# Performance work log

Hardware: AMD Instinct MI355X
Metric: run time of the kernel (lower is better)

The kernel has to match this reference:

```python
import jax, jax.numpy as jnp
import numpy as np

N = 50000
EPS = 1e-12


def sage_conv(x, src, dst, Wl, bl, Wr):
    # mean aggregation of source features into target nodes
    msg = x[src]                                            # [E, d]
    agg = jax.ops.segment_sum(msg, dst, num_segments=N)     # [N, d]
    cnt = jax.ops.segment_sum(jnp.ones_like(src, dtype=x.dtype), dst, num_segments=N)
    agg = agg / jnp.maximum(cnt, 1.0)[:, None]
    out = agg @ Wl + bl + x @ Wr                            # lin_l(aggr) + lin_r(x)
    # L2 normalize (PyG normalize=True)
    nrm = jnp.maximum(jnp.linalg.norm(out, axis=-1, keepdims=True), EPS)
    return out / nrm


def setup_inputs() -> dict:
    key = jax.random.key(0)
    ks = jax.random.split(key, 12)
    d_in, d_h, d_out = 128, 128, 40
    E = 800000
    x = jax.random.normal(ks[0], (N, d_in), dtype=jnp.float32)
    edge_index = jax.random.randint(ks[1], (2, E), 0, N, dtype=jnp.int64)

    def xavier(k, shp):
        lim = np.sqrt(6.0 / (shp[0] + shp[1]))
        return jax.random.uniform(k, shp, jnp.float32, -lim, lim)

    return {
        "x": x, "edge_index": edge_index,
        "W1l": xavier(ks[2], (d_in, d_h)), "b1": jnp.zeros((d_h,), jnp.float32), "W1r": xavier(ks[3], (d_in, d_h)),
        "W2l": xavier(ks[4], (d_h, d_h)),  "b2": jnp.zeros((d_h,), jnp.float32), "W2r": xavier(ks[5], (d_h, d_h)),
        "W3l": xavier(ks[6], (d_h, d_h)),  "b3": jnp.zeros((d_h,), jnp.float32), "W3r": xavier(ks[7], (d_h, d_h)),
        "Wfc": xavier(ks[8], (d_h, d_out)), "bfc": jnp.zeros((d_out,), jnp.float32),
    }


def reference(x, edge_index, W1l, b1, W1r, W2l, b2, W2r, W3l, b3, W3r, Wfc, bfc):
    src, dst = edge_index[0], edge_index[1]
    h = sage_conv(x, src, dst, W1l, b1, W1r)
    h = jax.nn.relu(h)                       # dropout = identity at eval
    h = sage_conv(h, src, dst, W2l, b2, W2r)
    h = jax.nn.relu(h)
    h = sage_conv(h, src, dst, W3l, b3, W3r)
    return jax.nn.softmax(h @ Wfc + bfc, axis=-1)
```

## Files before the change

### kernel.cpp

```cpp
#include <hip/hip_runtime.h>
#include <math.h>

#define NN 50000
#define D 128
#define NB 49
#define NBUK 256
#define EPB 4096

typedef __attribute__((ext_vector_type(8))) short bf16x8;
typedef __attribute__((ext_vector_type(4))) float f32x4;
typedef __attribute__((ext_vector_type(2))) float f32x2;

__device__ __forceinline__ float bf2f(unsigned short u) {
    union { unsigned int i; float f; } c;
    c.i = ((unsigned int)u) << 16;
    return c.f;
}
__device__ __forceinline__ unsigned short f2bf(float f) {
    union { float f; unsigned int i; } c;
    c.f = f;
    unsigned int u = c.i;
    return (unsigned short)((u + 0x7FFFu + ((u >> 16) & 1u)) >> 16);
}
__device__ __forceinline__ unsigned char f2f8(float v) {
    return (unsigned char)(__builtin_amdgcn_cvt_pk_fp8_f32(v, v, 0, false) & 0xFF);
}


__global__ __launch_bounds__(256) void f32_cvt_kernel(const float* __restrict__ src,
                                                      unsigned short* __restrict__ dstb,
                                                      unsigned int* __restrict__ dst8,
                                                      int n4) {
    int i = blockIdx.x * 256 + threadIdx.x;
    if (i < n4) {
        float4 v = ((const float4*)src)[i];
        ushort4 o;
        o.x = f2bf(v.x); o.y = f2bf(v.y); o.z = f2bf(v.z); o.w = f2bf(v.w);
        ((ushort4*)dstb)[i] = o;
        unsigned int p01 = __builtin_amdgcn_cvt_pk_fp8_f32(v.x, v.y, 0, false);
        unsigned int p23 = __builtin_amdgcn_cvt_pk_fp8_f32(v.z, v.w, 0, false);
        dst8[i] = (p01 & 0xFFFFu) | (p23 << 16);
    }
}


__global__ __launch_bounds__(256) void pack_all_kernel(const float* __restrict__ W0,
                                                       const float* __restrict__ W1,
                                                       const float* __restrict__ W2,
                                                       const float* __restrict__ W3,
                                                       const float* __restrict__ W4,
                                                       const float* __restrict__ W5,
                                                       unsigned short* __restrict__ P) {
    int i = blockIdx.x * 256 + threadIdx.x;
    int w = i >> 14, j = i & 16383;
    const float* W = (w == 0) ? W0 : (w == 1) ? W1 : (w == 2) ? W2
                   : (w == 3) ? W3 : (w == 4) ? W4 : W5;
    int e = j & 7, l = (j >> 3) & 63, n = (j >> 9) & 7, ks = j >> 12;
    int k = ks * 32 + (l >> 4) * 8 + e;
    int col = n * 16 + (l & 15);
    P[i] = f2bf(W[k * D + col]);
}


__global__ __launch_bounds__(256) void bucket_hist_kernel(const int* __restrict__ e, int E,
                                                          int* __restrict__ bukcnt) {
    __shared__ int h[NBUK];
    int t = threadIdx.x;
    h[t] = 0;
    __syncthreads();
    int base = blockIdx.x * EPB;
    #pragma unroll
    for (int k = 0; k < 4; ++k) {
        int idx = base + k * 1024 + t * 4;
        if (idx + 4 <= E) {
            int4 d = *(const int4*)(e + E + idx);
            atomicAdd(&h[d.x >> 8], 1);
            atomicAdd(&h[d.y >> 8], 1);
            atomicAdd(&h[d.z >> 8], 1);
            atomicAdd(&h[d.w >> 8], 1);
        } else {
            for (int i = idx; i < E; ++i) atomicAdd(&h[e[E + i] >> 8], 1);
        }
    }
    __syncthreads();
    if (h[t]) atomicAdd(&bukcnt[t], h[t]);
}

__global__ __launch_bounds__(256) void bucket_scan_kernel(const int* __restrict__ bukcnt,
                                                          int* __restrict__ bukbase,
                                                          int* __restrict__ bukfill, int E) {
    __shared__ int wsum[4], woff[4];
    int t = threadIdx.x;
    int lane = t & 63, wave = t >> 6;
    int v = bukcnt[t];
    int incl = v;
    for (int off = 1; off < 64; off <<= 1) {
        int u = __shfl_up(incl, off);
        if (lane >= off) incl += u;
    }
    if (lane == 63) wsum[wave] = incl;
    __syncthreads();
    if (t == 0) {
        int r = 0;
        #pragma unroll
        for (int w = 0; w < 4; ++w) { woff[w] = r; r += wsum[w]; }
    }
    __syncthreads();
    int excl = woff[wave] + incl - v;
    bukbase[t] = excl;
    bukfill[t] = excl;
    if (t == 255) bukbase[NBUK] = E;
}

__global__ __launch_bounds__(256) void bucket_scatter_kernel(const int* __restrict__ e, int E,
                                                             int* __restrict__ bukfill,
                                                             unsigned int* __restrict__ ebuk) {
    __shared__ int h[NBUK];
    __shared__ int res[NBUK];
    int t = threadIdx.x;
    h[t] = 0;
    __syncthreads();
    int base = blockIdx.x * EPB;
    int4 d[4];
    #pragma unroll
    for (int k = 0; k < 4; ++k) {
        int idx = base + k * 1024 + t * 4;
        if (idx + 4 <= E) {
            d[k] = *(const int4*)(e + E + idx);
        } else {
            d[k].x = (idx + 0 < E) ? e[E + idx + 0] : -1;
            d[k].y = (idx + 1 < E) ? e[E + idx + 1] : -1;
            d[k].z = (idx + 2 < E) ? e[E + idx + 2] : -1;
            d[k].w = (idx + 3 < E) ? e[E + idx + 3] : -1;
        }
        if (d[k].x >= 0) atomicAdd(&h[d[k].x >> 8], 1);
        if (d[k].y >= 0) atomicAdd(&h[d[k].y >> 8], 1);
        if (d[k].z >= 0) atomicAdd(&h[d[k].z >> 8], 1);
        if (d[k].w >= 0) atomicAdd(&h[d[k].w >> 8], 1);
    }
    __syncthreads();
    res[t] = h[t] ? atomicAdd(&bukfill[t], h[t]) : 0;
    h[t] = 0;
    __syncthreads();
    #pragma unroll
    for (int k = 0; k < 4; ++k) {
        int idx = base + k * 1024 + t * 4;
        int4 s;
        if (idx + 4 <= E) {
            s = *(const int4*)(e + idx);
        } else {
            s.x = (idx + 0 < E) ? e[idx + 0] : 0;
            s.y = (idx + 1 < E) ? e[idx + 1] : 0;
            s.z = (idx + 2 < E) ? e[idx + 2] : 0;
            s.w = (idx + 3 < E) ? e[idx + 3] : 0;
        }
        if (d[k].x >= 0) { int b = d[k].x >> 8; int r = atomicAdd(&h[b], 1);
            ebuk[res[b] + r] = (unsigned int)(s.x & 0xFFFF) | ((unsigned int)(d[k].x & 255) << 16); }
        if (d[k].y >= 0) { int b = d[k].y >> 8; int r = atomicAdd(&h[b], 1);
            ebuk[res[b] + r] = (unsigned int)(s.y & 0xFFFF) | ((unsigned int)(d[k].y & 255) << 16); }
        if (d[k].z >= 0) { int b = d[k].z >> 8; int r = atomicAdd(&h[b], 1);
            ebuk[res[b] + r] = (unsigned int)(s.z & 0xFFFF) | ((unsigned int)(d[k].z & 255) << 16); }
        if (d[k].w >= 0) { int b = d[k].w >> 8; int r = atomicAdd(&h[b], 1);
            ebuk[res[b] + r] = (unsigned int)(s.w & 0xFFFF) | ((unsigned int)(d[k].w & 255) << 16); }
    }
}

__global__ __launch_bounds__(256) void cnt_hist_kernel(const unsigned int* __restrict__ ebuk,
                                                       const int* __restrict__ bukbase,
                                                       int* __restrict__ cnt, int N) {
    __shared__ int c[NBUK];
    int t = threadIdx.x, b = blockIdx.x;
    c[t] = 0;
    __syncthreads();
    int lo = bukbase[b], hi = bukbase[b + 1];
    for (int i = lo + t; i < hi; i += 256) atomicAdd(&c[ebuk[i] >> 16], 1);
    __syncthreads();
    int g = b * NBUK + t;
    if (g < N) cnt[g] = c[t];
}

__global__ __launch_bounds__(256) void scan_blocks_kernel(const int* __restrict__ cnt,
                                                          int* __restrict__ row_ptr,
                                                          int* __restrict__ bsum, int N) {
    __shared__ int wsum[4], woff[4];
    int t = threadIdx.x;
    int lane = t & 63, wave = t >> 6;
    int base = blockIdx.x * 1024 + t * 4;
    int4 v = make_int4(0, 0, 0, 0);
    if (base + 4 <= N) v = *(const int4*)(cnt + base);
    int s = v.x + v.y + v.z + v.w;
    int incl = s;
    for (int off = 1; off < 64; off <<= 1) {
        int u = __shfl_up(incl, off);
        if (lane >= off) incl += u;
    }
    if (lane == 63) wsum[wave] = incl;
    __syncthreads();
    if (t == 0) {
        int r = 0;
        #pragma unroll
        for (int w = 0; w < 4; ++w) { woff[w] = r; r += wsum[w]; }
    }
    __syncthreads();
    int excl = woff[wave] + incl - s;
    if (base + 4 <= N) {
        int4 rp;
        rp.x = excl;
        rp.y = rp.x + v.x;
        rp.z = rp.y + v.y;
        rp.w = rp.z + v.z;
        *(int4*)(row_ptr + base) = rp;
    }
    if (t == 255) bsum[blockIdx.x] = woff[3] + wsum[3];
}

__global__ __launch_bounds__(64) void scan_bsums_kernel(int* __restrict__ bsum, int nb) {
    int l = threadIdx.x;
    int v = (l < nb) ? bsum[l] : 0;
    int incl = v;
    for (int off = 1; off < 64; off <<= 1) {
        int u = __shfl_up(incl, off);
        if (l >= off) incl += u;
    }
    if (l < nb) bsum[l] = incl - v;
}

__global__ __launch_bounds__(256) void scan_add_kernel(const int* __restrict__ cnt,
                                                       int* __restrict__ row_ptr,
                                                       const int* __restrict__ bsum,
                                                       float* __restrict__ inv_cnt,
                                                       int N, int E) {
    int base = blockIdx.x * 1024 + threadIdx.x * 4;
    int off = bsum[blockIdx.x];
    if (base + 4 <= N) {
        int4 rp = *(int4*)(row_ptr + base);
        rp.x += off; rp.y += off; rp.z += off; rp.w += off;
        *(int4*)(row_ptr + base) = rp;
        int4 c = *(const int4*)(cnt + base);
        float4 ic;
        ic.x = 1.0f / fmaxf((float)c.x, 1.0f);
        ic.y = 1.0f / fmaxf((float)c.y, 1.0f);
        ic.z = 1.0f / fmaxf((float)c.z, 1.0f);
        ic.w = 1.0f / fmaxf((float)c.w, 1.0f);
        *(float4*)(inv_cnt + base) = ic;
    }
    if (blockIdx.x == 0 && threadIdx.x == 0) row_ptr[N] = E;
}

__global__ __launch_bounds__(256) void csr_scatter_kernel(const unsigned int* __restrict__ ebuk,
                                                          const int* __restrict__ bukbase,
                                                          const int* __restrict__ row_ptr,
                                                          unsigned short* __restrict__ csr_src,
                                                          int N) {
    __shared__ int rp[NBUK];
    __shared__ int lf[NBUK];
    int t = threadIdx.x, b = blockIdx.x;
    int g = b * NBUK + t;
    rp[t] = (g < N) ? row_ptr[g] : 0;
    lf[t] = 0;
    __syncthreads();
    int lo = bukbase[b], hi = bukbase[b + 1];
    for (int i = lo + t; i < hi; i += 256) {
        unsigned int v = ebuk[i];
        int dl = v >> 16;
        int r = atomicAdd(&lf[dl], 1);
        csr_src[rp[dl] + r] = (unsigned short)(v & 0xFFFF);
    }
}


__device__ __forceinline__ void acc_f8(float& x, float& y, float& z, float& w,
                                       unsigned int v) {
    f32x2 lo = __builtin_amdgcn_cvt_pk_f32_fp8(v, false);
    f32x2 hi = __builtin_amdgcn_cvt_pk_f32_fp8(v, true);
    x += lo.x; y += lo.y; z += hi.x; w += hi.y;
}

__global__ __launch_bounds__(256) void aggregate_kernel(const unsigned int* __restrict__ h8,
                                                        const int* __restrict__ row_ptr,
                                                        const unsigned short* __restrict__ csr_src,
                                                        const float* __restrict__ inv_cnt,
                                                        unsigned short* __restrict__ agg, int N) {
    int node = (int)((blockIdx.x * blockDim.x + threadIdx.x) >> 5);
    int l = threadIdx.x & 31;
    if (node >= N) return;
    int beg = row_ptr[node], end = row_ptr[node + 1];
    float a0x = 0.f, a0y = 0.f, a0z = 0.f, a0w = 0.f;
    float a1x = 0.f, a1y = 0.f, a1z = 0.f, a1w = 0.f;
    for (int base = beg; base < end; base += 32) {
        int idx = 0;
        if (base + l < end) idx = csr_src[base + l];
        int n = min(32, end - base);
        int j = 0;
        for (; j + 8 <= n; j += 8) {
            int s0 = __shfl(idx, j + 0, 32);
            int s1 = __shfl(idx, j + 1, 32);
            int s2 = __shfl(idx, j + 2, 32);
            int s3 = __shfl(idx, j + 3, 32);
            int s4 = __shfl(idx, j + 4, 32);
            int s5 = __shfl(idx, j + 5, 32);
            int s6 = __shfl(idx, j + 6, 32);
            int s7 = __shfl(idx, j + 7, 32);
            unsigned int v0 = h8[(size_t)s0 * 32 + l];
            unsigned int v1 = h8[(size_t)s1 * 32 + l];
            unsigned int v2 = h8[(size_t)s2 * 32 + l];
            unsigned int v3 = h8[(size_t)s3 * 32 + l];
            unsigned int v4 = h8[(size_t)s4 * 32 + l];
            unsigned int v5 = h8[(size_t)s5 * 32 + l];
            unsigned int v6 = h8[(size_t)s6 * 32 + l];
            unsigned int v7 = h8[(size_t)s7 * 32 + l];
            acc_f8(a0x, a0y, a0z, a0w, v0);
            acc_f8(a1x, a1y, a1z, a1w, v1);
            acc_f8(a0x, a0y, a0z, a0w, v2);
            acc_f8(a1x, a1y, a1z, a1w, v3);
            acc_f8(a0x, a0y, a0z, a0w, v4);
            acc_f8(a1x, a1y, a1z, a1w, v5);
            acc_f8(a0x, a0y, a0z, a0w, v6);
            acc_f8(a1x, a1y, a1z, a1w, v7);
        }
        for (; j < n; ++j) {
            int s = __shfl(idx, j, 32);
            acc_f8(a0x, a0y, a0z, a0w, h8[(size_t)s * 32 + l]);
        }
    }
    float iv = inv_cnt[node];
    ushort4 o;
    o.x = f2bf((a0x + a1x) * iv);
    o.y = f2bf((a0y + a1y) * iv);
    o.z = f2bf((a0z + a1z) * iv);
    o.w = f2bf((a0w + a1w) * iv);
    ((ushort4*)agg)[(size_t)node * 32 + l] = o;
}


__global__ __launch_bounds__(256) void sage_mfma_kernel(const unsigned short* __restrict__ aggb,
                                                        const unsigned short* __restrict__ xb,
                                                        const unsigned short* __restrict__ wlp,
                                                        const unsigned short* __restrict__ wrp,
                                                        const float* __restrict__ bl,
                                                        unsigned short* __restrict__ outb,
                                                        unsigned char* __restrict__ out8,
                                                        float* __restrict__ outf,
                                                        int relu, int N) {
    int t = threadIdx.x;
    int w = t >> 6;
    int l = t & 63;
    int rlo = l & 15;
    int khi = l >> 4;
    int row0 = blockIdx.x * 64 + w * 16;
    int rowA = row0 + rlo;
    bool okA = rowA < N;

    f32x4 acc[8];
    #pragma unroll
    for (int n = 0; n < 8; ++n) {
        float b = bl[n * 16 + rlo];
        acc[n] = (f32x4){b, b, b, b};
    }

    const short* Ap = (const short*)aggb + (size_t)(okA ? rowA : 0) * D + khi * 8;
    const short* Xp = (const short*)xb   + (size_t)(okA ? rowA : 0) * D + khi * 8;
    const short* WL = (const short*)wlp + l * 8;
    const short* WR = (const short*)wrp + l * 8;
    const bf16x8 Z = {0, 0, 0, 0, 0, 0, 0, 0};

    #pragma unroll 1
    for (int ks = 0; ks < 4; ++ks) {
        bf16x8 a = okA ? *(const bf16x8*)(Ap + ks * 32) : Z;
        #pragma unroll
        for (int n = 0; n < 8; ++n) {
            bf16x8 b = *(const bf16x8*)(WL + (ks * 8 + n) * 512);
            acc[n] = __builtin_amdgcn_mfma_f32_16x16x32_bf16(a, b, acc[n], 0, 0, 0);
        }
    }
    #pragma unroll 1
    for (int ks = 0; ks < 4; ++ks) {
        bf16x8 a = okA ? *(const bf16x8*)(Xp + ks * 32) : Z;
        #pragma unroll
        for (int n = 0; n < 8; ++n) {
            bf16x8 b = *(const bf16x8*)(WR + (ks * 8 + n) * 512);
            acc[n] = __builtin_amdgcn_mfma_f32_16x16x32_bf16(a, b, acc[n], 0, 0, 0);
        }
    }

    #pragma unroll
    for (int r = 0; r < 4; ++r) {
        float s = 0.f;
        #pragma unroll
        for (int n = 0; n < 8; ++n) s += acc[n][r] * acc[n][r];
        s += __shfl_xor(s, 1);
        s += __shfl_xor(s, 2);
        s += __shfl_xor(s, 4);
        s += __shfl_xor(s, 8);
        float inv = 1.0f / fmaxf(sqrtf(s), 1e-12f);
        int gr = row0 + khi * 4 + r;
        if (gr < N) {
            if (outb) {
                #pragma unroll
                for (int n = 0; n < 8; ++n) {
                    float v = acc[n][r] * inv;
                    if (relu) v = fmaxf(v, 0.f);
                    outb[(size_t)gr * D + n * 16 + rlo] = f2bf(v);
                    out8[(size_t)gr * D + n * 16 + rlo] = f2f8(v);
                }
            } else {
                #pragma unroll
                for (int n = 0; n < 8; ++n) {
                    float v = acc[n][r] * inv;
                    outf[(size_t)gr * D + n * 16 + rlo] = v;
                }
            }
        }
    }
}


__global__ __launch_bounds__(256, 4) void fc_softmax_kernel(const float* __restrict__ h,
                                                            const float* __restrict__ Wfc,
                                                            const float* __restrict__ bfc,
                                                            float* __restrict__ out, int N) {
    __shared__ float sH[32 * 132];
    __shared__ float sW[128 * 40];
    __shared__ float sB[40];
    int t = threadIdx.x;
    int row0 = blockIdx.x * 32;

    const float4* W4 = (const float4*)Wfc;
    float4* sW4 = (float4*)sW;
    for (int i = t; i < 1280; i += 256) sW4[i] = W4[i];
    if (t < 40) sB[t] = bfc[t];

    const float4* h4 = (const float4*)h;
    for (int i = t; i < 32 * 32; i += 256) {
        int r = i >> 5, c = i & 31;
        int gr = row0 + r;
        float4 v = make_float4(0.f, 0.f, 0.f, 0.f);
        if (gr < N) v = h4[(size_t)gr * 32 + c];
        *(float4*)(sH + r * 132 + c * 4) = v;
    }
    __syncthreads();

    int r = t >> 3, sub = t & 7;
    int c0 = sub * 5;
    float acc[5];
    #pragma unroll
    for (int i = 0; i < 5; ++i) acc[i] = sB[c0 + i];

    const float* hr = sH + r * 132;
    for (int k = 0; k < 128; ++k) {
        float hv = hr[k];
        const float* wk = sW + k * 40 + c0;
        #pragma unroll
        for (int i = 0; i < 5; ++i) acc[i] += hv * wk[i];
    }

    float m = acc[0];
    #pragma unroll
    for (int i = 1; i < 5; ++i) m = fmaxf(m, acc[i]);
    for (int off = 1; off < 8; off <<= 1) m = fmaxf(m, __shfl_xor(m, off));
    float s = 0.f;
    #pragma unroll
    for (int i = 0; i < 5; ++i) { acc[i] = expf(acc[i] - m); s += acc[i]; }
    for (int off = 1; off < 8; off <<= 1) s += __shfl_xor(s, off);
    float inv = 1.0f / s;

    int gr = row0 + r;
    if (gr < N) {
        #pragma unroll
        for (int i = 0; i < 5; ++i) out[(size_t)gr * 40 + c0 + i] = acc[i] * inv;
    }
}


extern "C" void kernel_launch(void* const* d_in, const int* in_sizes, int n_in,
                              void* d_out, int out_size, void* d_ws, size_t ws_size,
                              hipStream_t stream) {
    const float* x   = (const float*)d_in[0];
    const int*   e   = (const int*)d_in[1];
    const float* W1l = (const float*)d_in[2];
    const float* b1  = (const float*)d_in[3];
    const float* W1r = (const float*)d_in[4];
    const float* W2l = (const float*)d_in[5];
    const float* b2  = (const float*)d_in[6];
    const float* W2r = (const float*)d_in[7];
    const float* W3l = (const float*)d_in[8];
    const float* b3  = (const float*)d_in[9];
    const float* W3r = (const float*)d_in[10];
    const float* Wfc = (const float*)d_in[11];
    const float* bfc = (const float*)d_in[12];
    float* out = (float*)d_out;

    const int N = NN;
    const int E = in_sizes[1] / 2;

    unsigned char* p = (unsigned char*)d_ws;
    unsigned short* xb   = (unsigned short*)p; p += (size_t)N * D * 2;
    unsigned short* h1b  = (unsigned short*)p; p += (size_t)N * D * 2;
    unsigned short* h2b  = (unsigned short*)p; p += (size_t)N * D * 2;
    unsigned short* aggb = (unsigned short*)p; p += (size_t)N * D * 2;
    unsigned char*  xf8  = (unsigned char*)p;  p += (size_t)N * D;
    unsigned char*  h1f8 = (unsigned char*)p;  p += (size_t)N * D;
    unsigned short* wpk  = (unsigned short*)p; p += 6 * 16384 * 2;
    float* inv_cnt = (float*)p; p += (size_t)N * 4;
    int* row_ptr = (int*)p; p += (size_t)(N + 4) * 4;
    int* cnt     = (int*)p; p += (size_t)N * 4;
    int* bukcnt  = (int*)p; p += NBUK * 4;
    int* bukbase = (int*)p; p += (NBUK + 4) * 4;
    int* bukfill = (int*)p; p += NBUK * 4;
    int* bsum    = (int*)p; p += 64 * 4;
    unsigned int* ebuk = (unsigned int*)p; p += (size_t)E * 4;
    unsigned short* csr_src = (unsigned short*)p;
    float* h3f = (float*)xb;
    unsigned char* h2f8 = xf8;

    unsigned short* w1lp = wpk;
    unsigned short* w1rp = wpk + 16384;
    unsigned short* w2lp = wpk + 2 * 16384;
    unsigned short* w2rp = wpk + 3 * 16384;
    unsigned short* w3lp = wpk + 4 * 16384;
    unsigned short* w3rp = wpk + 5 * 16384;

    hipMemsetAsync(bukcnt, 0, sizeof(int) * NBUK, stream);

    f32_cvt_kernel<<<(N * D / 4 + 255) / 256, 256, 0, stream>>>(x, xb, (unsigned int*)xf8,
                                                                N * D / 4);
    pack_all_kernel<<<384, 256, 0, stream>>>(W1l, W1r, W2l, W2r, W3l, W3r, wpk);

    int EB = (E + EPB - 1) / EPB;
    bucket_hist_kernel<<<EB, 256, 0, stream>>>(e, E, bukcnt);
    bucket_scan_kernel<<<1, 256, 0, stream>>>(bukcnt, bukbase, bukfill, E);
    bucket_scatter_kernel<<<EB, 256, 0, stream>>>(e, E, bukfill, ebuk);
    cnt_hist_kernel<<<NBUK, 256, 0, stream>>>(ebuk, bukbase, cnt, N);
    scan_blocks_kernel<<<NB, 256, 0, stream>>>(cnt, row_ptr, bsum, N);
    scan_bsums_kernel<<<1, 64, 0, stream>>>(bsum, NB);
    scan_add_kernel<<<NB, 256, 0, stream>>>(cnt, row_ptr, bsum, inv_cnt, N, E);
    csr_scatter_kernel<<<NBUK, 256, 0, stream>>>(ebuk, bukbase, row_ptr, csr_src, N);

    int aggBlocks = (N * 32 + 255) / 256;
    int sageBlocks = (N + 63) / 64;
    int fcBlocks = (N + 31) / 32;

    aggregate_kernel<<<aggBlocks, 256, 0, stream>>>((const unsigned int*)xf8, row_ptr,
                                                    csr_src, inv_cnt, aggb, N);
    sage_mfma_kernel<<<sageBlocks, 256, 0, stream>>>(aggb, xb, w1lp, w1rp, b1,
                                                     h1b, h1f8, nullptr, 1, N);

    aggregate_kernel<<<aggBlocks, 256, 0, stream>>>((const unsigned int*)h1f8, row_ptr,
                                                    csr_src, inv_cnt, aggb, N);
    sage_mfma_kernel<<<sageBlocks, 256, 0, stream>>>(aggb, h1b, w2lp, w2rp, b2,
                                                     h2b, h2f8, nullptr, 1, N);

    aggregate_kernel<<<aggBlocks, 256, 0, stream>>>((const unsigned int*)h2f8, row_ptr,
                                                    csr_src, inv_cnt, aggb, N);
    sage_mfma_kernel<<<sageBlocks, 256, 0, stream>>>(aggb, h2b, w3lp, w3rp, b3,
                                                     nullptr, nullptr, h3f, 0, N);

    fc_softmax_kernel<<<fcBlocks, 256, 0, stream>>>(h3f, Wfc, bfc, out, N);
}
```

Baseline: 204.0 us.

## Fuse preprocessing kernels, merge count/scan, and fold FC softmax into last SAGE layer

Merges the x conversion and weight packing into one launch. Replaces the separate count histogram and three-pass scan with a per-bucket count and local scan, using the bucket base as the offset. Fuses the final SAGE layer's normalized output straight into shared memory, where the FC and softmax run without the fp32 round trip to global memory. This cuts several kernel launches and about 25 MB of intermediate traffic, at the cost of more shared memory (about 54 KB) in the fused kernel, which may lower occupancy.

```diff
diff --git a/kernel.cpp b/kernel.cpp
--- a/kernel.cpp
+++ b/kernel.cpp
@@ -3,7 +3,6 @@
 
 #define NN 50000
 #define D 128
-#define NB 49
 #define NBUK 256
 #define EPB 4096
 
@@ -27,38 +26,38 @@
 }
 
 
-__global__ __launch_bounds__(256) void f32_cvt_kernel(const float* __restrict__ src,
-                                                      unsigned short* __restrict__ dstb,
-                                                      unsigned int* __restrict__ dst8,
-                                                      int n4) {
-    int i = blockIdx.x * 256 + threadIdx.x;
-    if (i < n4) {
-        float4 v = ((const float4*)src)[i];
-        ushort4 o;
-        o.x = f2bf(v.x); o.y = f2bf(v.y); o.z = f2bf(v.z); o.w = f2bf(v.w);
-        ((ushort4*)dstb)[i] = o;
-        unsigned int p01 = __builtin_amdgcn_cvt_pk_fp8_f32(v.x, v.y, 0, false);
-        unsigned int p23 = __builtin_amdgcn_cvt_pk_fp8_f32(v.z, v.w, 0, false);
-        dst8[i] = (p01 & 0xFFFFu) | (p23 << 16);
-    }
-}
-
-
-__global__ __launch_bounds__(256) void pack_all_kernel(const float* __restrict__ W0,
-                                                       const float* __restrict__ W1,
-                                                       const float* __restrict__ W2,
-                                                       const float* __restrict__ W3,
-                                                       const float* __restrict__ W4,
-                                                       const float* __restrict__ W5,
-                                                       unsigned short* __restrict__ P) {
-    int i = blockIdx.x * 256 + threadIdx.x;
-    int w = i >> 14, j = i & 16383;
-    const float* W = (w == 0) ? W0 : (w == 1) ? W1 : (w == 2) ? W2
-                   : (w == 3) ? W3 : (w == 4) ? W4 : W5;
-    int e = j & 7, l = (j >> 3) & 63, n = (j >> 9) & 7, ks = j >> 12;
-    int k = ks * 32 + (l >> 4) * 8 + e;
-    int col = n * 16 + (l & 15);
-    P[i] = f2bf(W[k * D + col]);
+__global__ __launch_bounds__(256) void cvtpack_kernel(const float* __restrict__ x,
+                                                      unsigned short* __restrict__ xb,
+                                                      unsigned int* __restrict__ x8,
+                                                      int n4,
+                                                      const float* __restrict__ W0,
+                                                      const float* __restrict__ W1,
+                                                      const float* __restrict__ W2,
+                                                      const float* __restrict__ W3,
+                                                      const float* __restrict__ W4,
+                                                      const float* __restrict__ W5,
+                                                      unsigned short* __restrict__ P) {
+    if (blockIdx.x < 384) {
+        int i = blockIdx.x * 256 + threadIdx.x;
+        int w = i >> 14, j = i & 16383;
+        const float* W = (w == 0) ? W0 : (w == 1) ? W1 : (w == 2) ? W2
+                       : (w == 3) ? W3 : (w == 4) ? W4 : W5;
+        int e = j & 7, l = (j >> 3) & 63, n = (j >> 9) & 7, ks = j >> 12;
+        int k = ks * 32 + (l >> 4) * 8 + e;
+        int col = n * 16 + (l & 15);
+        P[i] = f2bf(W[k * D + col]);
+    } else {
+        int i = (blockIdx.x - 384) * 256 + threadIdx.x;
+        if (i < n4) {
+            float4 v = ((const float4*)x)[i];
+            ushort4 o;
+            o.x = f2bf(v.x); o.y = f2bf(v.y); o.z = f2bf(v.z); o.w = f2bf(v.w);
+            ((ushort4*)xb)[i] = o;
+            unsigned int p01 = __builtin_amdgcn_cvt_pk_fp8_f32(v.x, v.y, 0, false);
+            unsigned int p23 = __builtin_amdgcn_cvt_pk_fp8_f32(v.z, v.w, 0, false);
+            x8[i] = (p01 & 0xFFFFu) | (p23 << 16);
+        }
+    }
 }
 
 
@@ -165,31 +164,23 @@
     }
 }
 
-__global__ __launch_bounds__(256) void cnt_hist_kernel(const unsigned int* __restrict__ ebuk,
+
+__global__ __launch_bounds__(256) void cnt_scan_kernel(const unsigned int* __restrict__ ebuk,
                                                        const int* __restrict__ bukbase,
-                                                       int* __restrict__ cnt, int N) {
+                                                       int* __restrict__ row_ptr,
+                                                       float* __restrict__ inv_cnt,
+                                                       int N, int E) {
     __shared__ int c[NBUK];
+    __shared__ int wsum[4], woff[4];
     int t = threadIdx.x, b = blockIdx.x;
     c[t] = 0;
     __syncthreads();
     int lo = bukbase[b], hi = bukbase[b + 1];
     for (int i = lo + t; i < hi; i += 256) atomicAdd(&c[ebuk[i] >> 16], 1);
     __syncthreads();
-    int g = b * NBUK + t;
-    if (g < N) cnt[g] = c[t];
-}
-
-__global__ __launch_bounds__(256) void scan_blocks_kernel(const int* __restrict__ cnt,
-                                                          int* __restrict__ row_ptr,
-                                                          int* __restrict__ bsum, int N) {
-    __shared__ int wsum[4], woff[4];
-    int t = threadIdx.x;
+    int v = c[t];
     int lane = t & 63, wave = t >> 6;
-    int base = blockIdx.x * 1024 + t * 4;
-    int4 v = make_int4(0, 0, 0, 0);
-    if (base + 4 <= N) v = *(const int4*)(cnt + base);
-    int s = v.x + v.y + v.z + v.w;
-    int incl = s;
+    int incl = v;
     for (int off = 1; off < 64; off <<= 1) {
         int u = __shfl_up(incl, off);
         if (lane >= off) incl += u;
@@ -202,49 +193,13 @@
         for (int w = 0; w < 4; ++w) { woff[w] = r; r += wsum[w]; }
     }
     __syncthreads();
-    int excl = woff[wave] + incl - s;
-    if (base + 4 <= N) {
-        int4 rp;
-        rp.x = excl;
-        rp.y = rp.x + v.x;
-        rp.z = rp.y + v.y;
-        rp.w = rp.z + v.z;
-        *(int4*)(row_ptr + base) = rp;
-    }
-    if (t == 255) bsum[blockIdx.x] = woff[3] + wsum[3];
-}
-
-__global__ __launch_bounds__(64) void scan_bsums_kernel(int* __restrict__ bsum, int nb) {
-    int l = threadIdx.x;
-    int v = (l < nb) ? bsum[l] : 0;
-    int incl = v;
-    for (int off = 1; off < 64; off <<= 1) {
-        int u = __shfl_up(incl, off);
-        if (l >= off) incl += u;
-    }
-    if (l < nb) bsum[l] = incl - v;
-}
-
-__global__ __launch_bounds__(256) void scan_add_kernel(const int* __restrict__ cnt,
-                                                       int* __restrict__ row_ptr,
-                                                       const int* __restrict__ bsum,
-                                                       float* __restrict__ inv_cnt,
-                                                       int N, int E) {
-    int base = blockIdx.x * 1024 + threadIdx.x * 4;
-    int off = bsum[blockIdx.x];
-    if (base + 4 <= N) {
-        int4 rp = *(int4*)(row_ptr + base);
-        rp.x += off; rp.y += off; rp.z += off; rp.w += off;
-        *(int4*)(row_ptr + base) = rp;
-        int4 c = *(const int4*)(cnt + base);
-        float4 ic;
-        ic.x = 1.0f / fmaxf((float)c.x, 1.0f);
-        ic.y = 1.0f / fmaxf((float)c.y, 1.0f);
-        ic.z = 1.0f / fmaxf((float)c.z, 1.0f);
-        ic.w = 1.0f / fmaxf((float)c.w, 1.0f);
-        *(float4*)(inv_cnt + base) = ic;
-    }
-    if (blockIdx.x == 0 && threadIdx.x == 0) row_ptr[N] = E;
+    int excl = woff[wave] + incl - v;
+    int g = b * NBUK + t;
+    if (g < N) {
+        row_ptr[g] = bukbase[b] + excl;
+        inv_cnt[g] = 1.0f / fmaxf((float)v, 1.0f);
+    }
+    if (g == N) row_ptr[N] = E;
 }
 
 __global__ __launch_bounds__(256) void csr_scatter_kernel(const unsigned int* __restrict__ ebuk,
@@ -340,8 +295,7 @@
                                                         const float* __restrict__ bl,
                                                         unsigned short* __restrict__ outb,
                                                         unsigned char* __restrict__ out8,
-                                                        float* __restrict__ outf,
-                                                        int relu, int N) {
+                                                        int N) {
     int t = threadIdx.x;
     int w = t >> 6;
     int l = t & 63;
@@ -395,79 +349,121 @@
         float inv = 1.0f / fmaxf(sqrtf(s), 1e-12f);
         int gr = row0 + khi * 4 + r;
         if (gr < N) {
-            if (outb) {
-                #pragma unroll
-                for (int n = 0; n < 8; ++n) {
-                    float v = acc[n][r] * inv;
-                    if (relu) v = fmaxf(v, 0.f);
-                    outb[(size_t)gr * D + n * 16 + rlo] = f2bf(v);
-                    out8[(size_t)gr * D + n * 16 + rlo] = f2f8(v);
-                }
-            } else {
-                #pragma unroll
-                for (int n = 0; n < 8; ++n) {
-                    float v = acc[n][r] * inv;
-                    outf[(size_t)gr * D + n * 16 + rlo] = v;
-                }
+            #pragma unroll
+            for (int n = 0; n < 8; ++n) {
+                float v = fmaxf(acc[n][r] * inv, 0.f);
+                outb[(size_t)gr * D + n * 16 + rlo] = f2bf(v);
+                out8[(size_t)gr * D + n * 16 + rlo] = f2f8(v);
             }
         }
     }
 }
 
 
-__global__ __launch_bounds__(256, 4) void fc_softmax_kernel(const float* __restrict__ h,
-                                                            const float* __restrict__ Wfc,
-                                                            const float* __restrict__ bfc,
-                                                            float* __restrict__ out, int N) {
-    __shared__ float sH[32 * 132];
+__global__ __launch_bounds__(256) void sage_mfma_fc_kernel(const unsigned short* __restrict__ aggb,
+                                                           const unsigned short* __restrict__ xb,
+                                                           const unsigned short* __restrict__ wlp,
+                                                           const unsigned short* __restrict__ wrp,
+                                                           const float* __restrict__ bl,
+                                                           const float* __restrict__ Wfc,
+                                                           const float* __restrict__ bfc,
+                                                           float* __restrict__ out, int N) {
+    __shared__ float sH[64 * 132];
     __shared__ float sW[128 * 40];
     __shared__ float sB[40];
     int t = threadIdx.x;
-    int row0 = blockIdx.x * 32;
-
-    const float4* W4 = (const float4*)Wfc;
-    float4* sW4 = (float4*)sW;
-    for (int i = t; i < 1280; i += 256) sW4[i] = W4[i];
-    if (t < 40) sB[t] = bfc[t];
-
-    const float4* h4 = (const float4*)h;
-    for (int i = t; i < 32 * 32; i += 256) {
-        int r = i >> 5, c = i & 31;
-        int gr = row0 + r;
-        float4 v = make_float4(0.f, 0.f, 0.f, 0.f);
-        if (gr < N) v = h4[(size_t)gr * 32 + c];
-        *(float4*)(sH + r * 132 + c * 4) = v;
-    }
-    __syncthreads();
-
-    int r = t >> 3, sub = t & 7;
-    int c0 = sub * 5;
-    float acc[5];
-    #pragma unroll
-    for (int i = 0; i < 5; ++i) acc[i] = sB[c0 + i];
-
-    const float* hr = sH + r * 132;
+    int w = t >> 6;
+    int l = t & 63;
+    int rlo = l & 15;
+    int khi = l >> 4;
+    int row0 = blockIdx.x * 64 + w * 16;
+    int rowA = row0 + rlo;
+    bool okA = rowA < N;
+
+    {
+        const float4* W4 = (const float4*)Wfc;
+        float4* sW4 = (float4*)sW;
+        for (int i = t; i < 1280; i += 256) sW4[i] = W4[i];
+        if (t < 40) sB[t] = bfc[t];
+    }
+
+    f32x4 acc[8];
+    #pragma unroll
+    for (int n = 0; n < 8; ++n) {
+        float b = bl[n * 16 + rlo];
+        acc[n] = (f32x4){b, b, b, b};
+    }
+
+    const short* Ap = (const short*)aggb + (size_t)(okA ? rowA : 0) * D + khi * 8;
+    const short* Xp = (const short*)xb   + (size_t)(okA ? rowA : 0) * D + khi * 8;
+    const short* WL = (const short*)wlp + l * 8;
+    const short* WR = (const short*)wrp + l * 8;
+    const bf16x8 Z = {0, 0, 0, 0, 0, 0, 0, 0};
+
+    #pragma unroll 1
+    for (int ks = 0; ks < 4; ++ks) {
+        bf16x8 a = okA ? *(const bf16x8*)(Ap + ks * 32) : Z;
+        #pragma unroll
+        for (int n = 0; n < 8; ++n) {
+            bf16x8 b = *(const bf16x8*)(WL + (ks * 8 + n) * 512);
+            acc[n] = __builtin_amdgcn_mfma_f32_16x16x32_bf16(a, b, acc[n], 0, 0, 0);
+        }
+    }
+    #pragma unroll 1
+    for (int ks = 0; ks < 4; ++ks) {
+        bf16x8 a = okA ? *(const bf16x8*)(Xp + ks * 32) : Z;
+        #pragma unroll
+        for (int n = 0; n < 8; ++n) {
+            bf16x8 b = *(const bf16x8*)(WR + (ks * 8 + n) * 512);
+            acc[n] = __builtin_amdgcn_mfma_f32_16x16x32_bf16(a, b, acc[n], 0, 0, 0);
+        }
+    }
+
+    #pragma unroll
+    for (int r = 0; r < 4; ++r) {
+        float s = 0.f;
+        #pragma unroll
+        for (int n = 0; n < 8; ++n) s += acc[n][r] * acc[n][r];
+        s += __shfl_xor(s, 1);
+        s += __shfl_xor(s, 2);
+        s += __shfl_xor(s, 4);
+        s += __shfl_xor(s, 8);
+        float inv = 1.0f / fmaxf(sqrtf(s), 1e-12f);
+        int lr = w * 16 + khi * 4 + r;
+        #pragma unroll
+        for (int n = 0; n < 8; ++n)
+            sH[lr * 132 + n * 16 + rlo] = acc[n][r] * inv;
+    }
+    __syncthreads();
+
+    int r2 = t >> 2, sub = t & 3;
+    int c0 = sub * 10;
+    float fa[10];
+    #pragma unroll
+    for (int i = 0; i < 10; ++i) fa[i] = sB[c0 + i];
+    const float* hr = sH + r2 * 132;
     for (int k = 0; k < 128; ++k) {
         float hv = hr[k];
         const float* wk = sW + k * 40 + c0;
         #pragma unroll
-        for (int i = 0; i < 5; ++i) acc[i] += hv * wk[i];
-    }
-
-    float m = acc[0];
-    #pragma unroll
-    for (int i = 1; i < 5; ++i) m = fmaxf(m, acc[i]);
-    for (int off = 1; off < 8; off <<= 1) m = fmaxf(m, __shfl_xor(m, off));
-    float s = 0.f;
-    #pragma unroll
-    for (int i = 0; i < 5; ++i) { acc[i] = expf(acc[i] - m); s += acc[i]; }
-    for (int off = 1; off < 8; off <<= 1) s += __shfl_xor(s, off);
-    float inv = 1.0f / s;
-
-    int gr = row0 + r;
+        for (int i = 0; i < 10; ++i) fa[i] += hv * wk[i];
+    }
+    float m = fa[0];
+    #pragma unroll
+    for (int i = 1; i < 10; ++i) m = fmaxf(m, fa[i]);
+    m = fmaxf(m, __shfl_xor(m, 1));
+    m = fmaxf(m, __shfl_xor(m, 2));
+    float ssum = 0.f;
+    #pragma unroll
+    for (int i = 0; i < 10; ++i) { fa[i] = expf(fa[i] - m); ssum += fa[i]; }
+    ssum += __shfl_xor(ssum, 1);
+    ssum += __shfl_xor(ssum, 2);
+    float inv = 1.0f / ssum;
+
+    int gr = blockIdx.x * 64 + r2;
     if (gr < N) {
         #pragma unroll
-        for (int i = 0; i < 5; ++i) out[(size_t)gr * 40 + c0 + i] = acc[i] * inv;
+        for (int i = 0; i < 10; ++i) out[(size_t)gr * 40 + c0 + i] = fa[i] * inv;
     }
 }
 
@@ -503,14 +499,11 @@
     unsigned short* wpk  = (unsigned short*)p; p += 6 * 16384 * 2;
     float* inv_cnt = (float*)p; p += (size_t)N * 4;
     int* row_ptr = (int*)p; p += (size_t)(N + 4) * 4;
-    int* cnt     = (int*)p; p += (size_t)N * 4;
     int* bukcnt  = (int*)p; p += NBUK * 4;
     int* bukbase = (int*)p; p += (NBUK + 4) * 4;
     int* bukfill = (int*)p; p += NBUK * 4;
-    int* bsum    = (int*)p; p += 64 * 4;
     unsigned int* ebuk = (unsigned int*)p; p += (size_t)E * 4;
     unsigned short* csr_src = (unsigned short*)p;
-    float* h3f = (float*)xb;
     unsigned char* h2f8 = xf8;
 
     unsigned short* w1lp = wpk;
@@ -522,38 +515,32 @@
 
     hipMemsetAsync(bukcnt, 0, sizeof(int) * NBUK, stream);
 
-    f32_cvt_kernel<<<(N * D / 4 + 255) / 256, 256, 0, stream>>>(x, xb, (unsigned int*)xf8,
-                                                                N * D / 4);
-    pack_all_kernel<<<384, 256, 0, stream>>>(W1l, W1r, W2l, W2r, W3l, W3r, wpk);
+    int n4 = N * D / 4;
+    cvtpack_kernel<<<384 + (n4 + 255) / 256, 256, 0, stream>>>(
+        x, xb, (unsigned int*)xf8, n4, W1l, W1r, W2l, W2r, W3l, W3r, wpk);
 
     int EB = (E + EPB - 1) / EPB;
     bucket_hist_kernel<<<EB, 256, 0, stream>>>(e, E, bukcnt);
     bucket_scan_kernel<<<1, 256, 0, stream>>>(bukcnt, bukbase, bukfill, E);
     bucket_scatter_kernel<<<EB, 256, 0, stream>>>(e, E, bukfill, ebuk);
-    cnt_hist_kernel<<<NBUK, 256, 0, stream>>>(ebuk, bukbase, cnt, N);
-    scan_blocks_kernel<<<NB, 256, 0, stream>>>(cnt, row_ptr, bsum, N);
-    scan_bsums_kernel<<<1, 64, 0, stream>>>(bsum, NB);
-    scan_add_kernel<<<NB, 256, 0, stream>>>(cnt, row_ptr, bsum, inv_cnt, N, E);
+    cnt_scan_kernel<<<NBUK, 256, 0, stream>>>(ebuk, bukbase, row_ptr, inv_cnt, N, E);
     csr_scatter_kernel<<<NBUK, 256, 0, stream>>>(ebuk, bukbase, row_ptr, csr_src, N);
 
     int aggBlocks = (N * 32 + 255) / 256;
     int sageBlocks = (N + 63) / 64;
-    int fcBlocks = (N + 31) / 32;
 
     aggregate_kernel<<<aggBlocks, 256, 0, stream>>>((const unsigned int*)xf8, row_ptr,
                                                     csr_src, inv_cnt, aggb, N);
     sage_mfma_kernel<<<sageBlocks, 256, 0, stream>>>(aggb, xb, w1lp, w1rp, b1,
-                                                     h1b, h1f8, nullptr, 1, N);
+                                                     h1b, h1f8, N);
 
     aggregate_kernel<<<aggBlocks, 256, 0, stream>>>((const unsigned int*)h1f8, row_ptr,
                                                     csr_src, inv_cnt, aggb, N);
     sage_mfma_kernel<<<sageBlocks, 256, 0, stream>>>(aggb, h1b, w2lp, w2rp, b2,
-                                                     h2b, h2f8, nullptr, 1, N);
+                                                     h2b, h2f8, N);
 
     aggregate_kernel<<<aggBlocks, 256, 0, stream>>>((const unsigned int*)h2f8, row_ptr,
                                                     csr_src, inv_cnt, aggb, N);
-    sage_mfma_kernel<<<sageBlocks, 256, 0, stream>>>(aggb, h2b, w3lp, w3rp, b3,
-                                                     nullptr, nullptr, h3f, 0, N);
-
-    fc_softmax_kernel<<<fcBlocks, 256, 0, stream>>>(h3f, Wfc, bfc, out, N);
-}
+    sage_mfma_fc_kernel<<<sageBlocks, 256, 0, stream>>>(aggb, h2b, w3lp, w3rp, b3,
+                                                        Wfc, bfc, out, N);
+}
```

Measured after the change: 193.9 us. -4.9%, faster.
